# Optimization experiments

Measured on AMD Instinct MI355X. Metric: run time of the kernel, lower is better.

The kernel has to match this reference:

```python
import jax, jax.numpy as jnp
import numpy as np

EPS = 1e-8  # torch F.cosine_similarity default eps


def setup_inputs() -> dict:
    key = jax.random.key(0)
    k1, k2, k3, k4 = jax.random.split(key, 4)
    B, S, D_in, D_e, E = 4, 128, 768, 256, 100000
    return {
        "x": jax.random.normal(k1, (B, S, D_in), dtype=jnp.float32),
        "W": jax.random.normal(k2, (D_e, D_in), dtype=jnp.float32) * 0.02,
        "b": jax.random.normal(k3, (D_e,), dtype=jnp.float32) * 0.02,
        "entity_embedding": jax.random.normal(k4, (E, D_e), dtype=jnp.float32),
    }


def reference(x, W, b, entity_embedding):
    # Linear projection + tanh: [B,S,D_e]
    q = jnp.tanh(jnp.einsum('bsi,ei->bse', x, W) + b)
    # Cosine similarity = L2-normalize both sides, then GEMM (fused; avoids
    # the [B,S,E,D] broadcast intermediate of the original).
    qn = q / jnp.maximum(jnp.linalg.norm(q, axis=-1, keepdims=True), EPS)
    en = entity_embedding / jnp.maximum(
        jnp.linalg.norm(entity_embedding, axis=-1, keepdims=True), EPS)
    return jnp.einsum('bsd,ed->bse', qn, en)  # [B,S,E]
```

## Files before the change

### kernel.cpp

```cpp
#include <hip/hip_runtime.h>
#include <hip/hip_bf16.h>

#define D_IN  768
#define D_E   256
#define M_TOT 512
#define E_TOT 100000

typedef __attribute__((ext_vector_type(4))) float f32x4;
typedef __attribute__((ext_vector_type(8))) short bf16x8;

__device__ __forceinline__ unsigned short bf16bits(float f) {
    union { __hip_bfloat16 h; unsigned short u; } c;
    c.h = __float2bfloat16(f);
    return c.u;
}

__device__ __forceinline__ void gload_lds16(const void* g, void* l) {
    __builtin_amdgcn_global_load_lds(
        (const __attribute__((address_space(1))) void*)g,
        (__attribute__((address_space(3))) void*)l, 16, 0, 0);
}

#define PROJ_BLOCKS 64
#define PREP_BLOCKS 1563
#define PP_GRID (PROJ_BLOCKS + PREP_BLOCKS)
#define PTM 8
#define PBK 64
#define PROUNDS (D_IN / PBK)

__global__ __launch_bounds__(512) void fused_pp(
    const float* __restrict__ x, const float* __restrict__ W,
    const float* __restrict__ b, const float* __restrict__ en,
    unsigned short* __restrict__ qb, unsigned short* __restrict__ eb)
{
    __shared__ float ws[D_E * (PBK + 1)];
    __shared__ float xs[PTM][PBK];
    __shared__ float red[PTM][4];
    __shared__ float qiv[PTM];

    const int t   = threadIdx.x;
    const int bid = blockIdx.x;

    if (bid >= PROJ_BLOCKS) {
        const int lane = t & 63;
        const int gw   = (bid - PROJ_BLOCKS) * 8 + (t >> 6);
        #pragma unroll 2
        for (int i = 0; i < 8; ++i) {
            const int row = gw * 8 + i;
            if (row >= E_TOT) break;
            const float4 v = *reinterpret_cast<const float4*>(
                en + (size_t)row * D_E + lane * 4);
            float s = v.x*v.x + v.y*v.y + v.z*v.z + v.w*v.w;
            #pragma unroll
            for (int off = 1; off < 64; off <<= 1) s += __shfl_xor(s, off, 64);
            const float sc = 1.0f / fmaxf(sqrtf(s), 1e-8f);
            union { unsigned short u[4]; uint2 d; } o;
            o.u[0] = bf16bits(v.x * sc); o.u[1] = bf16bits(v.y * sc);
            o.u[2] = bf16bits(v.z * sc); o.u[3] = bf16bits(v.w * sc);
            *reinterpret_cast<uint2*>(eb + (size_t)row * D_E + lane * 4) = o.d;
        }
        return;
    }

    const int m0   = bid * PTM;
    const int e    = t & 255;
    const int half = t >> 8;
    const int c4   = t & 15;
    const int rr   = t >> 4;

    float4 wreg[8];
    float  xreg = 0.f;
    float  acc[4] = {0.f, 0.f, 0.f, 0.f};

    #pragma unroll
    for (int i = 0; i < 8; ++i)
        wreg[i] = *reinterpret_cast<const float4*>(
            &W[(size_t)(i * 32 + rr) * D_IN + c4 * 4]);
    xreg = x[(size_t)(m0 + (t >> 6)) * D_IN + (t & 63)];

    for (int rd = 0; rd < PROUNDS; ++rd) {
        #pragma unroll
        for (int i = 0; i < 8; ++i) {
            float* dst = &ws[(i * 32 + rr) * (PBK + 1) + c4 * 4];
            dst[0] = wreg[i].x; dst[1] = wreg[i].y;
            dst[2] = wreg[i].z; dst[3] = wreg[i].w;
        }
        xs[t >> 6][t & 63] = xreg;
        __syncthreads();
        if (rd + 1 < PROUNDS) {
            const int k0 = (rd + 1) * PBK;
            #pragma unroll
            for (int i = 0; i < 8; ++i)
                wreg[i] = *reinterpret_cast<const float4*>(
                    &W[(size_t)(i * 32 + rr) * D_IN + k0 + c4 * 4]);
            xreg = x[(size_t)(m0 + (t >> 6)) * D_IN + k0 + (t & 63)];
        }
        #pragma unroll
        for (int k = 0; k < PBK; ++k) {
            const float wv = ws[e * (PBK + 1) + k];
            #pragma unroll
            for (int j = 0; j < 4; ++j)
                acc[j] = fmaf(xs[half * 4 + j][k], wv, acc[j]);
        }
        __syncthreads();
    }

    const float bias = b[e];
    const int wv4 = (t >> 6) & 3;
    const int lane = t & 63;
    float q[4];
    #pragma unroll
    for (int j = 0; j < 4; ++j) {
        q[j] = tanhf(acc[j] + bias);
        float s = q[j] * q[j];
        #pragma unroll
        for (int off = 1; off < 64; off <<= 1) s += __shfl_xor(s, off, 64);
        if (lane == 0) red[half * 4 + j][wv4] = s;
    }
    __syncthreads();
    if (t < PTM) {
        const float s = red[t][0] + red[t][1] + red[t][2] + red[t][3];
        qiv[t] = 1.0f / fmaxf(sqrtf(s), 1e-8f);
    }
    __syncthreads();
    #pragma unroll
    for (int j = 0; j < 4; ++j)
        qb[(size_t)(m0 + half * 4 + j) * D_E + e] =
            bf16bits(q[j] * qiv[half * 4 + j]);
}

#define BM 128
#define BN 64
#define TPB 25
#define NGRPN 63
#define SIM_GRID (NGRPN * (M_TOT / BM))

__device__ __forceinline__ void stage_etile(
    const unsigned short* __restrict__ eb, int n0, unsigned short* dst, int t)
{
    #pragma unroll
    for (int i = 0; i < 4; ++i) {
        const int c   = i * 512 + t;
        const int row = c >> 5;
        const int c16 = c & 31;
        int rg = n0 + row;
        if (rg >= E_TOT) rg = E_TOT - 1;
        const unsigned short* src =
            eb + (size_t)rg * D_E + ((c16 ^ (row & 7)) << 3);
        gload_lds16(src, (void*)&dst[(size_t)c << 3]);
    }
}

__global__ __launch_bounds__(512, 2) void sim_kernel(
    const unsigned short* __restrict__ eb, const unsigned short* __restrict__ qb,
    float* __restrict__ out)
{
    __shared__ unsigned short qs[BM * D_E];
    __shared__ unsigned short es[3][BN * D_E];

    const int t    = threadIdx.x;
    const int lane = t & 63;
    const int wid  = t >> 6;
    const int l15  = lane & 15;
    const int lk   = lane >> 4;
    const int wm   = (wid >> 1) * 32;
    const int wn   = (wid & 1) * 32;

    int vbid;
    {
        const int q = SIM_GRID >> 3, r = SIM_GRID & 7;
        const int xcd = blockIdx.x & 7, rk = blockIdx.x >> 3;
        vbid = (xcd < r ? xcd * (q + 1) : r * (q + 1) + (xcd - r) * q) + rk;
    }
    const int mg    = vbid & 3;
    const int ngrp  = vbid >> 2;
    const int m0    = mg * BM;
    const int nbase = ngrp * (TPB * BN);

    #pragma unroll
    for (int i = 0; i < 8; ++i) {
        const int c   = i * 512 + t;
        const int row = c >> 5;
        const int c16 = c & 31;
        const unsigned short* src =
            qb + (size_t)(m0 + row) * D_E + ((c16 ^ (row & 7)) << 3);
        gload_lds16(src, (void*)&qs[(size_t)c << 3]);
    }
    stage_etile(eb, nbase,      &es[0][0], t);
    stage_etile(eb, nbase + BN, &es[1][0], t);

    asm volatile("s_waitcnt vmcnt(8)" ::: "memory");
    __builtin_amdgcn_s_barrier();
    __builtin_amdgcn_sched_barrier(0);

    const char* qsb = reinterpret_cast<const char*>(qs);
    bf16x8 qf[2][8];
    #pragma unroll
    for (int mf = 0; mf < 2; ++mf) {
        const int rq = wm + mf * 16 + l15;
        #pragma unroll
        for (int ks = 0; ks < 8; ++ks) {
            const int cbq = (ks * 64 + lk * 16) ^ ((rq & 7) << 4);
            qf[mf][ks] = *reinterpret_cast<const bf16x8*>(qsb + rq * 512 + cbq);
        }
    }

    int cur = 0;
    for (int tt = 0; tt < TPB; ++tt) {
        const int n0 = nbase + tt * BN;
        if (n0 >= E_TOT) break;

        if (tt == 0)      asm volatile("s_waitcnt vmcnt(4)"  ::: "memory");
        else if (tt == 1) asm volatile("s_waitcnt vmcnt(8)"  ::: "memory");
        else              asm volatile("s_waitcnt vmcnt(12)" ::: "memory");
        __builtin_amdgcn_s_barrier();
        __builtin_amdgcn_sched_barrier(0);

        int nx = cur + 2; if (nx >= 3) nx -= 3;
        stage_etile(eb, n0 + 2 * BN, &es[nx][0], t);

        const char* esb = reinterpret_cast<const char*>(&es[cur][0]);

        f32x4 acc[2][2];
        #pragma unroll
        for (int mf = 0; mf < 2; ++mf)
            #pragma unroll
            for (int nf = 0; nf < 2; ++nf)
                acc[mf][nf] = (f32x4){0.f, 0.f, 0.f, 0.f};

        __builtin_amdgcn_s_setprio(1);
        #pragma unroll
        for (int ks = 0; ks < 8; ++ks) {
            const int kb = ks * 64 + lk * 16;
            bf16x8 ef[2];
            #pragma unroll
            for (int nf = 0; nf < 2; ++nf) {
                const int row = wn + nf * 16 + l15;
                const int cb  = kb ^ ((row & 7) << 4);
                ef[nf] = *reinterpret_cast<const bf16x8*>(esb + row * 512 + cb);
            }
            #pragma unroll
            for (int mf = 0; mf < 2; ++mf) {
                acc[mf][0] = __builtin_amdgcn_mfma_f32_16x16x32_bf16(
                    ef[0], qf[mf][ks], acc[mf][0], 0, 0, 0);
                acc[mf][1] = __builtin_amdgcn_mfma_f32_16x16x32_bf16(
                    ef[1], qf[mf][ks], acc[mf][1], 0, 0, 0);
            }
        }
        __builtin_amdgcn_s_setprio(0);

        #pragma unroll
        for (int mf = 0; mf < 2; ++mf) {
            const int m = m0 + wm + mf * 16 + l15;
            #pragma unroll
            for (int nf = 0; nf < 2; ++nf) {
                const int n = n0 + wn + nf * 16 + lk * 4;
                if (n < E_TOT)
                    *reinterpret_cast<f32x4*>(&out[(size_t)m * E_TOT + n]) =
                        acc[mf][nf];
            }
        }

        cur = (cur + 1 == 3) ? 0 : cur + 1;
    }
}

extern "C" void kernel_launch(void* const* d_in, const int* in_sizes, int n_in,
                              void* d_out, int out_size, void* d_ws, size_t ws_size,
                              hipStream_t stream) {
    const float* x  = (const float*)d_in[0];
    const float* W  = (const float*)d_in[1];
    const float* b  = (const float*)d_in[2];
    const float* en = (const float*)d_in[3];
    float* out = (float*)d_out;

    unsigned short* qb = (unsigned short*)d_ws;
    unsigned short* eb = (unsigned short*)((char*)d_ws + (size_t)M_TOT * D_E * 2);

    fused_pp<<<PP_GRID, 512, 0, stream>>>(x, W, b, en, qb, eb);
    sim_kernel<<<SIM_GRID, 512, 0, stream>>>(eb, qb, out);
}
```

Before: 138.6 us.

## Retile similarity GEMM to 32x512 blocks with per-wave K-pipelined staging and LDS-staged stores

Replaces the 128x64 persistent-loop tiling (25 N tiles per block, triple-buffered shared E tiles) with one 32x512 output tile per block. Each wave owns 64 entity rows and streams them in four K-chunks through a private double buffer. The accumulators are then written through swizzled LDS so each row is stored as contiguous 2KB runs. The aim is better-coalesced output writes, which dominate this output-bound kernel, and more blocks for parallelism. In exchange each entity row is now reloaded by 16 M-groups instead of 4, raising L2 traffic.

```diff
diff --git a/kernel.cpp b/kernel.cpp
--- a/kernel.cpp
+++ b/kernel.cpp
@@ -129,25 +129,24 @@
             bf16bits(q[j] * qiv[half * 4 + j]);
 }
 
-#define BM 128
-#define BN 64
-#define TPB 25
-#define NGRPN 63
-#define SIM_GRID (NGRPN * (M_TOT / BM))
-
-__device__ __forceinline__ void stage_etile(
-    const unsigned short* __restrict__ eb, int n0, unsigned short* dst, int t)
+#define SBM 32
+#define SBN 512
+#define NGN 196
+#define SIM_GRID (16 * NGN)
+
+__device__ __forceinline__ void stage_piece(
+    const unsigned short* __restrict__ eb, int nw, int kk,
+    unsigned short* dst, int lane)
 {
     #pragma unroll
-    for (int i = 0; i < 4; ++i) {
-        const int c   = i * 512 + t;
-        const int row = c >> 5;
-        const int c16 = c & 31;
-        int rg = n0 + row;
+    for (int i = 0; i < 8; ++i) {
+        const int c  = i * 64 + lane;
+        const int n  = c >> 3;
+        const int c8 = c & 7;
+        int rg = nw + n;
         if (rg >= E_TOT) rg = E_TOT - 1;
-        const unsigned short* src =
-            eb + (size_t)rg * D_E + ((c16 ^ (row & 7)) << 3);
-        gload_lds16(src, (void*)&dst[(size_t)c << 3]);
+        gload_lds16(eb + (size_t)rg * D_E + kk * 64 + ((c8 ^ (n & 7)) << 3),
+                    (void*)&dst[c * 8]);
     }
 }
 
@@ -155,113 +154,120 @@
     const unsigned short* __restrict__ eb, const unsigned short* __restrict__ qb,
     float* __restrict__ out)
 {
-    __shared__ unsigned short qs[BM * D_E];
-    __shared__ unsigned short es[3][BN * D_E];
+    __shared__ unsigned short pool[65536];
 
     const int t    = threadIdx.x;
     const int lane = t & 63;
-    const int wid  = t >> 6;
+    const int w    = t >> 6;
     const int l15  = lane & 15;
     const int lk   = lane >> 4;
-    const int wm   = (wid >> 1) * 32;
-    const int wn   = (wid & 1) * 32;
-
-    int vbid;
-    {
-        const int q = SIM_GRID >> 3, r = SIM_GRID & 7;
-        const int xcd = blockIdx.x & 7, rk = blockIdx.x >> 3;
-        vbid = (xcd < r ? xcd * (q + 1) : r * (q + 1) + (xcd - r) * q) + rk;
-    }
-    const int mg    = vbid & 3;
-    const int ngrp  = vbid >> 2;
-    const int m0    = mg * BM;
-    const int nbase = ngrp * (TPB * BN);
-
-    #pragma unroll
-    for (int i = 0; i < 8; ++i) {
+
+    const int vbid = (blockIdx.x & 7) * (SIM_GRID / 8) + (blockIdx.x >> 3);
+    const int mg = vbid & 15;
+    const int ng = vbid >> 4;
+    const int m0 = mg * SBM;
+    const int n0 = ng * SBN;
+    const int nw = n0 + w * 64;
+
+    char* poolb = reinterpret_cast<char*>(pool);
+
+    #pragma unroll
+    for (int i = 0; i < 2; ++i) {
         const int c   = i * 512 + t;
         const int row = c >> 5;
         const int c16 = c & 31;
-        const unsigned short* src =
-            qb + (size_t)(m0 + row) * D_E + ((c16 ^ (row & 7)) << 3);
-        gload_lds16(src, (void*)&qs[(size_t)c << 3]);
-    }
-    stage_etile(eb, nbase,      &es[0][0], t);
-    stage_etile(eb, nbase + BN, &es[1][0], t);
-
-    asm volatile("s_waitcnt vmcnt(8)" ::: "memory");
-    __builtin_amdgcn_s_barrier();
+        gload_lds16(qb + (size_t)(m0 + row) * D_E + ((c16 ^ (row & 7)) << 3),
+                    (void*)&pool[c * 8]);
+    }
+    asm volatile("s_waitcnt vmcnt(0)" ::: "memory");
     __builtin_amdgcn_sched_barrier(0);
-
-    const char* qsb = reinterpret_cast<const char*>(qs);
+    __builtin_amdgcn_s_barrier();
+
     bf16x8 qf[2][8];
     #pragma unroll
     for (int mf = 0; mf < 2; ++mf) {
-        const int rq = wm + mf * 16 + l15;
+        const int rq = mf * 16 + l15;
         #pragma unroll
         for (int ks = 0; ks < 8; ++ks) {
-            const int cbq = (ks * 64 + lk * 16) ^ ((rq & 7) << 4);
-            qf[mf][ks] = *reinterpret_cast<const bf16x8*>(qsb + rq * 512 + cbq);
-        }
-    }
-
-    int cur = 0;
-    for (int tt = 0; tt < TPB; ++tt) {
-        const int n0 = nbase + tt * BN;
-        if (n0 >= E_TOT) break;
-
-        if (tt == 0)      asm volatile("s_waitcnt vmcnt(4)"  ::: "memory");
-        else if (tt == 1) asm volatile("s_waitcnt vmcnt(8)"  ::: "memory");
-        else              asm volatile("s_waitcnt vmcnt(12)" ::: "memory");
-        __builtin_amdgcn_s_barrier();
+            const int cb = (ks * 64 + lk * 16) ^ ((l15 & 7) << 4);
+            qf[mf][ks] = *reinterpret_cast<const bf16x8*>(poolb + rq * 512 + cb);
+        }
+    }
+    asm volatile("s_waitcnt lgkmcnt(0)" ::: "memory");
+    __builtin_amdgcn_sched_barrier(0);
+    __builtin_amdgcn_s_barrier();
+
+    unsigned short* es0 = pool + w * 8192;
+    unsigned short* es1 = pool + w * 8192 + 4096;
+    const char* esb0 = reinterpret_cast<const char*>(es0);
+    const char* esb1 = reinterpret_cast<const char*>(es1);
+
+    stage_piece(eb, nw, 0, es0, lane);
+    stage_piece(eb, nw, 1, es1, lane);
+
+    f32x4 acc[2][4];
+    #pragma unroll
+    for (int mf = 0; mf < 2; ++mf)
+        #pragma unroll
+        for (int nf = 0; nf < 4; ++nf)
+            acc[mf][nf] = (f32x4){0.f, 0.f, 0.f, 0.f};
+
+    #pragma unroll
+    for (int kk = 0; kk < 4; ++kk) {
+        if (kk < 3) asm volatile("s_waitcnt vmcnt(8)" ::: "memory");
+        else        asm volatile("s_waitcnt vmcnt(0)" ::: "memory");
         __builtin_amdgcn_sched_barrier(0);
 
-        int nx = cur + 2; if (nx >= 3) nx -= 3;
-        stage_etile(eb, n0 + 2 * BN, &es[nx][0], t);
-
-        const char* esb = reinterpret_cast<const char*>(&es[cur][0]);
-
-        f32x4 acc[2][2];
-        #pragma unroll
-        for (int mf = 0; mf < 2; ++mf)
-            #pragma unroll
-            for (int nf = 0; nf < 2; ++nf)
-                acc[mf][nf] = (f32x4){0.f, 0.f, 0.f, 0.f};
-
-        __builtin_amdgcn_s_setprio(1);
-        #pragma unroll
-        for (int ks = 0; ks < 8; ++ks) {
-            const int kb = ks * 64 + lk * 16;
-            bf16x8 ef[2];
-            #pragma unroll
-            for (int nf = 0; nf < 2; ++nf) {
-                const int row = wn + nf * 16 + l15;
-                const int cb  = kb ^ ((row & 7) << 4);
-                ef[nf] = *reinterpret_cast<const bf16x8*>(esb + row * 512 + cb);
+        const char* esb = (kk & 1) ? esb1 : esb0;
+        #pragma unroll
+        for (int s = 0; s < 2; ++s) {
+            const int ks = kk * 2 + s;
+            bf16x8 ef[4];
+            #pragma unroll
+            for (int nf = 0; nf < 4; ++nf) {
+                const int n = nf * 16 + l15;
+                const int cb = (s * 64 + lk * 16) ^ ((n & 7) << 4);
+                ef[nf] = *reinterpret_cast<const bf16x8*>(esb + n * 128 + cb);
             }
             #pragma unroll
-            for (int mf = 0; mf < 2; ++mf) {
-                acc[mf][0] = __builtin_amdgcn_mfma_f32_16x16x32_bf16(
-                    ef[0], qf[mf][ks], acc[mf][0], 0, 0, 0);
-                acc[mf][1] = __builtin_amdgcn_mfma_f32_16x16x32_bf16(
-                    ef[1], qf[mf][ks], acc[mf][1], 0, 0, 0);
-            }
-        }
-        __builtin_amdgcn_s_setprio(0);
-
-        #pragma unroll
-        for (int mf = 0; mf < 2; ++mf) {
-            const int m = m0 + wm + mf * 16 + l15;
-            #pragma unroll
-            for (int nf = 0; nf < 2; ++nf) {
-                const int n = n0 + wn + nf * 16 + lk * 4;
-                if (n < E_TOT)
-                    *reinterpret_cast<f32x4*>(&out[(size_t)m * E_TOT + n]) =
-                        acc[mf][nf];
-            }
-        }
-
-        cur = (cur + 1 == 3) ? 0 : cur + 1;
+            for (int mf = 0; mf < 2; ++mf)
+                #pragma unroll
+                for (int nf = 0; nf < 4; ++nf)
+                    acc[mf][nf] = __builtin_amdgcn_mfma_f32_16x16x32_bf16(
+                        ef[nf], qf[mf][ks], acc[mf][nf], 0, 0, 0);
+        }
+        __builtin_amdgcn_sched_barrier(0);
+        if (kk == 0) stage_piece(eb, nw, 2, es0, lane);
+        if (kk == 1) stage_piece(eb, nw, 3, es1, lane);
+    }
+
+    __builtin_amdgcn_s_barrier();
+
+    #pragma unroll
+    for (int mf = 0; mf < 2; ++mf) {
+        const int mrow = mf * 16 + l15;
+        #pragma unroll
+        for (int nf = 0; nf < 4; ++nf) {
+            const int cc = w * 16 + nf * 4 + lk;
+            *reinterpret_cast<f32x4*>(
+                poolb + mrow * 2048 + ((cc ^ (mrow & 7)) << 4)) = acc[mf][nf];
+        }
+    }
+    asm volatile("s_waitcnt lgkmcnt(0)" ::: "memory");
+    __builtin_amdgcn_sched_barrier(0);
+    __builtin_amdgcn_s_barrier();
+
+    #pragma unroll
+    for (int j = 0; j < 8; ++j) {
+        const int c    = j * 512 + t;
+        const int rrow = c >> 7;
+        const int cc   = c & 127;
+        const f32x4 v = *reinterpret_cast<const f32x4*>(
+            poolb + rrow * 2048 + ((cc ^ (rrow & 7)) << 4));
+        const int n = n0 + cc * 4;
+        if (n < E_TOT)
+            *reinterpret_cast<f32x4*>(
+                &out[(size_t)(m0 + rrow) * E_TOT + n]) = v;
     }
 }
 
```

New measurement: 148.8 us. 7.4% more time.

## Retile similarity GEMM to 64x128 tiles with K-split pipelined staging

Applied to the files above, without the earlier changes.

Changes the similarity kernel from 128x64 output tiles to 64x128 tiles. The entity tile is streamed in four K-slices of 64 through a triple-buffered LDS ring, and accumulation runs across the slices, with output written after every fourth piece. LDS use per block shrinks, so launch bounds rise to four blocks per CU and the grid becomes 488 blocks with a simpler XCD mapping. The aim is higher occupancy and finer-grained load/compute overlap. In exchange there are more barriers per output tile, and the waitcnt bookkeeping is hand-tuned and brittle.

```diff
diff --git a/kernel.cpp b/kernel.cpp
--- a/kernel.cpp
+++ b/kernel.cpp
@@ -129,67 +129,63 @@
             bf16bits(q[j] * qiv[half * 4 + j]);
 }
 
-#define BM 128
-#define BN 64
-#define TPB 25
-#define NGRPN 63
-#define SIM_GRID (NGRPN * (M_TOT / BM))
-
-__device__ __forceinline__ void stage_etile(
-    const unsigned short* __restrict__ eb, int n0, unsigned short* dst, int t)
+#define TPB 13
+#define NP (TPB * 4)
+#define NGRPS 61
+#define SIM_GRID (NGRPS * 8)
+
+__device__ __forceinline__ void stage_piece(
+    const unsigned short* __restrict__ eb, int nbase, int g,
+    unsigned short* dst, int t)
 {
+    const int kk  = g & 3;
+    const int nt0 = nbase + (g >> 2) * 128;
+    #pragma unroll
+    for (int i = 0; i < 2; ++i) {
+        const int c  = i * 512 + t;
+        const int n  = c >> 3;
+        const int c8 = c & 7;
+        int rg = nt0 + n;
+        if (rg >= E_TOT) rg = E_TOT - 1;
+        gload_lds16(eb + (size_t)rg * D_E + kk * 64 + ((c8 ^ (n & 7)) << 3),
+                    (void*)&dst[(size_t)c << 3]);
+    }
+}
+
+__global__ __launch_bounds__(512, 4) void sim_kernel(
+    const unsigned short* __restrict__ eb, const unsigned short* __restrict__ qb,
+    float* __restrict__ out)
+{
+    __shared__ unsigned short qs[64 * D_E];
+    __shared__ unsigned short es[3][128 * 64];
+
+    const int t    = threadIdx.x;
+    const int lane = t & 63;
+    const int w    = t >> 6;
+    const int l15  = lane & 15;
+    const int lk   = lane >> 4;
+    const int wm   = (w >> 2) * 32;
+    const int wn   = (w & 3) * 32;
+
+    const int vbid = (blockIdx.x & 7) * NGRPS + (blockIdx.x >> 3);
+    const int mg    = vbid & 7;
+    const int ngrp  = vbid >> 3;
+    const int m0    = mg * 64;
+    const int nbase = ngrp * (TPB * 128);
+
     #pragma unroll
     for (int i = 0; i < 4; ++i) {
         const int c   = i * 512 + t;
         const int row = c >> 5;
         const int c16 = c & 31;
-        int rg = n0 + row;
-        if (rg >= E_TOT) rg = E_TOT - 1;
-        const unsigned short* src =
-            eb + (size_t)rg * D_E + ((c16 ^ (row & 7)) << 3);
-        gload_lds16(src, (void*)&dst[(size_t)c << 3]);
-    }
-}
-
-__global__ __launch_bounds__(512, 2) void sim_kernel(
-    const unsigned short* __restrict__ eb, const unsigned short* __restrict__ qb,
-    float* __restrict__ out)
-{
-    __shared__ unsigned short qs[BM * D_E];
-    __shared__ unsigned short es[3][BN * D_E];
-
-    const int t    = threadIdx.x;
-    const int lane = t & 63;
-    const int wid  = t >> 6;
-    const int l15  = lane & 15;
-    const int lk   = lane >> 4;
-    const int wm   = (wid >> 1) * 32;
-    const int wn   = (wid & 1) * 32;
-
-    int vbid;
-    {
-        const int q = SIM_GRID >> 3, r = SIM_GRID & 7;
-        const int xcd = blockIdx.x & 7, rk = blockIdx.x >> 3;
-        vbid = (xcd < r ? xcd * (q + 1) : r * (q + 1) + (xcd - r) * q) + rk;
-    }
-    const int mg    = vbid & 3;
-    const int ngrp  = vbid >> 2;
-    const int m0    = mg * BM;
-    const int nbase = ngrp * (TPB * BN);
-
-    #pragma unroll
-    for (int i = 0; i < 8; ++i) {
-        const int c   = i * 512 + t;
-        const int row = c >> 5;
-        const int c16 = c & 31;
-        const unsigned short* src =
-            qb + (size_t)(m0 + row) * D_E + ((c16 ^ (row & 7)) << 3);
-        gload_lds16(src, (void*)&qs[(size_t)c << 3]);
-    }
-    stage_etile(eb, nbase,      &es[0][0], t);
-    stage_etile(eb, nbase + BN, &es[1][0], t);
-
-    asm volatile("s_waitcnt vmcnt(8)" ::: "memory");
+        gload_lds16(qb + (size_t)(m0 + row) * D_E + ((c16 ^ (row & 7)) << 3),
+                    (void*)&qs[(size_t)c << 3]);
+    }
+    stage_piece(eb, nbase, 0, &es[0][0], t);
+    stage_piece(eb, nbase, 1, &es[1][0], t);
+
+    asm volatile("s_waitcnt vmcnt(4)" ::: "memory");
+    __builtin_amdgcn_sched_barrier(0);
     __builtin_amdgcn_s_barrier();
     __builtin_amdgcn_sched_barrier(0);
 
@@ -200,68 +196,74 @@
         const int rq = wm + mf * 16 + l15;
         #pragma unroll
         for (int ks = 0; ks < 8; ++ks) {
-            const int cbq = (ks * 64 + lk * 16) ^ ((rq & 7) << 4);
-            qf[mf][ks] = *reinterpret_cast<const bf16x8*>(qsb + rq * 512 + cbq);
-        }
-    }
-
-    int cur = 0;
-    for (int tt = 0; tt < TPB; ++tt) {
-        const int n0 = nbase + tt * BN;
-        if (n0 >= E_TOT) break;
-
-        if (tt == 0)      asm volatile("s_waitcnt vmcnt(4)"  ::: "memory");
-        else if (tt == 1) asm volatile("s_waitcnt vmcnt(8)"  ::: "memory");
-        else              asm volatile("s_waitcnt vmcnt(12)" ::: "memory");
+            const int cb = (ks * 64 + lk * 16) ^ ((rq & 7) << 4);
+            qf[mf][ks] = *reinterpret_cast<const bf16x8*>(qsb + rq * 512 + cb);
+        }
+    }
+
+    f32x4 acc[2][2];
+
+    #pragma unroll 1
+    for (int g = 0; g < NP; ++g) {
+        if (g == NP - 1)                asm volatile("s_waitcnt vmcnt(0)" ::: "memory");
+        else if (g >= 4 && (g & 3) < 2) asm volatile("s_waitcnt vmcnt(6)" ::: "memory");
+        else                            asm volatile("s_waitcnt vmcnt(2)" ::: "memory");
+        __builtin_amdgcn_sched_barrier(0);
         __builtin_amdgcn_s_barrier();
         __builtin_amdgcn_sched_barrier(0);
 
-        int nx = cur + 2; if (nx >= 3) nx -= 3;
-        stage_etile(eb, n0 + 2 * BN, &es[nx][0], t);
-
-        const char* esb = reinterpret_cast<const char*>(&es[cur][0]);
-
-        f32x4 acc[2][2];
-        #pragma unroll
-        for (int mf = 0; mf < 2; ++mf)
-            #pragma unroll
-            for (int nf = 0; nf < 2; ++nf)
-                acc[mf][nf] = (f32x4){0.f, 0.f, 0.f, 0.f};
+        if (g + 2 < NP)
+            stage_piece(eb, nbase, g + 2, &es[(g + 2) % 3][0], t);
+
+        if ((g & 3) == 0) {
+            #pragma unroll
+            for (int mf = 0; mf < 2; ++mf)
+                #pragma unroll
+                for (int nf = 0; nf < 2; ++nf)
+                    acc[mf][nf] = (f32x4){0.f, 0.f, 0.f, 0.f};
+        }
+
+        const char* esb = reinterpret_cast<const char*>(&es[g % 3][0]);
+
+        bf16x8 ef[2][2];
+        #pragma unroll
+        for (int nf = 0; nf < 2; ++nf) {
+            const int n = wn + nf * 16 + l15;
+            #pragma unroll
+            for (int s = 0; s < 2; ++s) {
+                const int cb = (s * 64 + lk * 16) ^ ((n & 7) << 4);
+                ef[nf][s] = *reinterpret_cast<const bf16x8*>(esb + n * 128 + cb);
+            }
+        }
 
         __builtin_amdgcn_s_setprio(1);
         #pragma unroll
-        for (int ks = 0; ks < 8; ++ks) {
-            const int kb = ks * 64 + lk * 16;
-            bf16x8 ef[2];
-            #pragma unroll
-            for (int nf = 0; nf < 2; ++nf) {
-                const int row = wn + nf * 16 + l15;
-                const int cb  = kb ^ ((row & 7) << 4);
-                ef[nf] = *reinterpret_cast<const bf16x8*>(esb + row * 512 + cb);
-            }
+        for (int s = 0; s < 2; ++s) {
+            const int ksg = (g & 3) * 2 + s;
             #pragma unroll
             for (int mf = 0; mf < 2; ++mf) {
                 acc[mf][0] = __builtin_amdgcn_mfma_f32_16x16x32_bf16(
-                    ef[0], qf[mf][ks], acc[mf][0], 0, 0, 0);
+                    ef[0][s], qf[mf][ksg], acc[mf][0], 0, 0, 0);
                 acc[mf][1] = __builtin_amdgcn_mfma_f32_16x16x32_bf16(
-                    ef[1], qf[mf][ks], acc[mf][1], 0, 0, 0);
+                    ef[1][s], qf[mf][ksg], acc[mf][1], 0, 0, 0);
             }
         }
         __builtin_amdgcn_s_setprio(0);
 
-        #pragma unroll
-        for (int mf = 0; mf < 2; ++mf) {
-            const int m = m0 + wm + mf * 16 + l15;
-            #pragma unroll
-            for (int nf = 0; nf < 2; ++nf) {
-                const int n = n0 + wn + nf * 16 + lk * 4;
-                if (n < E_TOT)
-                    *reinterpret_cast<f32x4*>(&out[(size_t)m * E_TOT + n]) =
-                        acc[mf][nf];
+        if ((g & 3) == 3) {
+            const int nt0 = nbase + (g >> 2) * 128;
+            #pragma unroll
+            for (int mf = 0; mf < 2; ++mf) {
+                const int m = m0 + wm + mf * 16 + l15;
+                #pragma unroll
+                for (int nf = 0; nf < 2; ++nf) {
+                    const int n = nt0 + wn + nf * 16 + lk * 4;
+                    if (n < E_TOT)
+                        *reinterpret_cast<f32x4*>(
+                            &out[(size_t)m * E_TOT + n]) = acc[mf][nf];
+                }
             }
         }
-
-        cur = (cur + 1 == 3) ? 0 : cur + 1;
     }
 }
 
```

New measurement: 254.0 us. +83.2%, slower.
